# Kernel tuning notes

Hardware: AMD Instinct MI355X
Metric: run time of the kernel (lower is better)

The kernel has to match this reference:

```python
import jax, jax.numpy as jnp
import numpy as np

B, NE, NI, D = 256, 1024, 1024, 256  # batch, E cells, I cells, patch dim (16x16)
K_GAIN, N_EXP = 0.04, 2.0            # power-law i/o: k * relu(I)**n
TAU_E, TAU_I, DT = 0.02, 0.01, 0.001
STEPS, LAST_N = 200, 50              # int(T/dt) with T=0.2; average last 50 states
S_EE0, S_EI0, S_IE0, S_II0 = 3.75, 1.86, 3.13, 1.11 - 0.02
EPS = 1e-12
JEE, JEI, JIE, JII = 0.044, 0.023, 0.042, 0.018
SIGMA = 32.0


def ring_kernel(n_post, n_pre, sigma=SIGMA):
    post = np.linspace(0.0, 180.0, n_post + 1)[:-1]
    pre = np.linspace(0.0, 180.0, n_pre + 1)[:-1]
    d = np.abs(post[:, None] - pre[None, :])
    d = np.minimum(d, 180.0 - d)
    return np.exp(-(d * d) / (2.0 * sigma * sigma)).astype(np.float32)


def setup_inputs() -> dict:
    key = jax.random.key(0)
    kx, kE, kI = jax.random.split(key, 3)
    x_batch = jax.random.uniform(kx, (B, D), dtype=jnp.float32)
    W_EE = JEE * ring_kernel(NE, NE)
    np.fill_diagonal(W_EE, 0.0)
    W_EI = JEI * ring_kernel(NE, NI)
    W_IE = JIE * ring_kernel(NI, NE)
    W_II = JII * ring_kernel(NI, NI)
    np.fill_diagonal(W_II, 0.0)
    Wff_E = 0.1 * jax.random.uniform(kE, (NE, D), dtype=jnp.float32)
    Wff_E = Wff_E / (jnp.linalg.norm(Wff_E, axis=1, keepdims=True) + 1e-8)
    Wff_I = 0.1 * jax.random.uniform(kI, (NI, D), dtype=jnp.float32)
    Wff_I = Wff_I / (jnp.linalg.norm(Wff_I, axis=1, keepdims=True) + 1e-8)
    return {
        'x_batch': x_batch,
        'W_EE': jnp.asarray(W_EE), 'W_EI': jnp.asarray(W_EI),
        'W_IE': jnp.asarray(W_IE), 'W_II': jnp.asarray(W_II),
        'Wff_E': Wff_E, 'Wff_I': Wff_I,
    }


def powerlaw_io(I):
    return K_GAIN * jnp.maximum(I, 0.0) ** N_EXP


def reference(x_batch, W_EE, W_EI, W_IE, W_II, Wff_E, Wff_I):
    # per-postsynaptic current scalers (computed under no_grad in torch)
    gE_E = jax.lax.stop_gradient(S_EE0 / (W_EE.sum(axis=1) + EPS))
    gI_E = jax.lax.stop_gradient(S_EI0 / (W_EI.sum(axis=1) + EPS))
    gE_I = jax.lax.stop_gradient(S_IE0 / (W_IE.sum(axis=1) + EPS))
    gI_I = jax.lax.stop_gradient(S_II0 / (W_II.sum(axis=1) + EPS))
    # in-place clamp + rescale of weights (as in forward_dynamics)
    W_EE = jnp.minimum(W_EE, 0.15) * gE_E[:, None]
    W_EI = jnp.maximum(W_EI, 0.0005) * gI_E[:, None]
    W_IE = W_IE * gE_I[:, None]
    W_II = W_II * gI_I[:, None]

    Iff_E = x_batch @ Wff_E.T  # (B, nE)
    Iff_I = x_batch @ Wff_I.T  # (B, nI)

    def step(carry, t):
        rE, rI, accE, accI = carry
        IE = Iff_E + rE @ W_EE.T - rI @ W_EI.T
        II = Iff_I + rE @ W_IE.T - rI @ W_II.T
        rE = rE + (DT / TAU_E) * (-rE + powerlaw_io(IE))
        rI = rI + (DT / TAU_I) * (-rI + powerlaw_io(II))
        w = (t >= STEPS - LAST_N).astype(rE.dtype)
        return (rE, rI, accE + w * rE, accI + w * rI), None

    z = jnp.zeros((B, NE), dtype=x_batch.dtype)
    zi = jnp.zeros((B, NI), dtype=x_batch.dtype)
    (rE, rI, accE, accI), _ = jax.lax.scan(step, (z, zi, z, zi), jnp.arange(STEPS))
    rE_bar = accE / LAST_N
    rI_bar = accI / LAST_N
    return (rE_bar, rI_bar)
```

## Files before the change

### kernel.cpp

```cpp
#include <hip/hip_runtime.h>
#include <stdint.h>

typedef __attribute__((ext_vector_type(8))) _Float16 f16x8;
typedef __attribute__((ext_vector_type(8))) unsigned short u16x8;
typedef __attribute__((ext_vector_type(4))) float f32x4;

__device__ __forceinline__ float bf2f(unsigned short u) {
    union { uint32_t u; float f; } v; v.u = ((uint32_t)u) << 16; return v.f;
}
__device__ __forceinline__ unsigned short f2h(float f) {
    _Float16 h = (_Float16)f;
    return __builtin_bit_cast(unsigned short, h);
}
__device__ __forceinline__ f32x4 MFMAH(u16x8 a, u16x8 b, f32x4 c) {
    return __builtin_amdgcn_mfma_f32_16x16x32_f16(
        __builtin_bit_cast(f16x8, a), __builtin_bit_cast(f16x8, b), c, 0, 0, 0);
}

__device__ __forceinline__ int is_f32(const void* p) {
    const uint32_t* u = (const uint32_t*)p;
    int c = 0;
    #pragma unroll
    for (int i = 0; i < 64; i++) c += (u[i] >> 15) & 1;
    return c >= 4;
}
__device__ __forceinline__ float load_any(const void* base, size_t idx, int f32) {
    return f32 ? ((const float*)base)[idx] : bf2f(((const unsigned short*)base)[idx]);
}

__global__ void zero_kernel(float* __restrict__ p) {
    p[(size_t)blockIdx.x * 256 + threadIdx.x] = 0.0f;
}

__global__ void conv_kernel(const void* __restrict__ src, unsigned short* __restrict__ dst,
                            int clamp_wei) {
    int f32 = is_f32(src);
    size_t base = ((size_t)blockIdx.x * 256 + threadIdx.x) * 8;
    unsigned short v[8];
    if (f32) {
        const float* s = (const float*)src + base;
        #pragma unroll
        for (int e = 0; e < 8; e++) {
            float f = s[e];
            if (clamp_wei) f = fmaxf(f, 0.0005f);
            v[e] = f2h(f);
        }
    } else {
        const unsigned short* s = (const unsigned short*)src + base;
        #pragma unroll
        for (int e = 0; e < 8; e++) {
            float f = bf2f(s[e]);
            if (clamp_wei) f = fmaxf(f, 0.0005f);
            v[e] = f2h(f);
        }
    }
    *(u16x8*)(dst + base) = *(u16x8*)v;
}

__global__ void g_kernel(const void* __restrict__ WEE, const void* __restrict__ WEI,
                         const void* __restrict__ WIE, const void* __restrict__ WII,
                         float* __restrict__ gE, float* __restrict__ gI) {
    int i = blockIdx.x;
    int tid = threadIdx.x;
    const void* TE; const void* TI; float sEc, sIc; size_t row;
    if (i < 1024) { TE = WEE; TI = WEI; sEc = 3.75f; sIc = 1.86f; row = i; }
    else          { TE = WIE; TI = WII; sEc = 3.13f; sIc = (float)(1.11 - 0.02); row = i - 1024; }
    int fE = is_f32(TE), fI = is_f32(TI);
    float se = 0.f, si = 0.f;
    for (int j = tid; j < 1024; j += 256) {
        se += load_any(TE, row * 1024 + j, fE);
        si += load_any(TI, row * 1024 + j, fI);
    }
    for (int o = 32; o > 0; o >>= 1) { se += __shfl_down(se, o); si += __shfl_down(si, o); }
    __shared__ float lsE[4], lsI[4];
    int w = tid >> 6;
    if ((tid & 63) == 0) { lsE[w] = se; lsI[w] = si; }
    __syncthreads();
    if (tid == 0) {
        float te = lsE[0] + lsE[1] + lsE[2] + lsE[3];
        float ti = lsI[0] + lsI[1] + lsI[2] + lsI[3];
        gE[i] = sEc / (te + 1e-12f);
        gI[i] = sIc / (ti + 1e-12f);
    }
}

__global__ __launch_bounds__(256) void iff_kernel(const unsigned short* __restrict__ x,
                                                  const unsigned short* __restrict__ WffE,
                                                  const unsigned short* __restrict__ WffI,
                                                  float* __restrict__ Iff) {
    int n0 = blockIdx.x * 32;
    int m0 = blockIdx.y * 64;
    int tid = threadIdx.x, w = tid >> 6, lane = tid & 63;
    int l15 = lane & 15, quad = lane >> 4;
    int arow = m0 + 16 * w + l15;
    int nA = n0 + l15, nB = n0 + 16 + l15;
    const unsigned short* bA = (nA < 1024) ? (WffE + (size_t)nA * 256) : (WffI + (size_t)(nA - 1024) * 256);
    const unsigned short* bB = (nB < 1024) ? (WffE + (size_t)nB * 256) : (WffI + (size_t)(nB - 1024) * 256);
    f32x4 acc0 = {0.f, 0.f, 0.f, 0.f}, acc1 = {0.f, 0.f, 0.f, 0.f};
    #pragma unroll
    for (int ks = 0; ks < 8; ks++) {
        int k = ks * 32 + quad * 8;
        u16x8 a  = *(const u16x8*)(x + (size_t)arow * 256 + k);
        u16x8 b0 = *(const u16x8*)(bA + k);
        u16x8 b1 = *(const u16x8*)(bB + k);
        acc0 = MFMAH(a, b0, acc0);
        acc1 = MFMAH(a, b1, acc1);
    }
    #pragma unroll
    for (int v = 0; v < 4; v++) {
        int row = m0 + 16 * w + quad * 4 + v;
        Iff[(size_t)row * 2048 + n0 + l15]      = acc0[v];
        Iff[(size_t)row * 2048 + n0 + 16 + l15] = acc1[v];
    }
}

#define FLAG_STRIDE 32
__global__ __launch_bounds__(256, 1) void persist_kernel(
    const unsigned short* __restrict__ WEEc, const unsigned short* __restrict__ WEIc,
    const unsigned short* __restrict__ WIEc, const unsigned short* __restrict__ WIIc,
    unsigned short* __restrict__ h0, unsigned short* __restrict__ h1,
    const float* __restrict__ Iff, const float* __restrict__ gE, const float* __restrict__ gI,
    float* __restrict__ out, int* __restrict__ flags)
{
    __shared__ unsigned short Wl[32 * 2048];
    int bid = blockIdx.x;
    int nT = bid & 63;
    int mT = bid >> 6;
    int n0 = nT * 32;
    int m0 = mT * 64;
    int tid = threadIdx.x, w = tid >> 6, lane = tid & 63;
    int l15 = lane & 15, quad = lane >> 4;

    bool isEblk = (n0 < 1024);
    const unsigned short* W0 = isEblk ? WEEc : WIEc;
    const unsigned short* W1 = isEblk ? WEIc : WIIc;
    int nbase = n0 & 1023;

    {
        int k = tid * 8;
        const unsigned short* s0 = W0 + (size_t)nbase * 1024;
        const unsigned short* s1 = W1 + (size_t)nbase * 1024;
        #pragma unroll 4
        for (int row = 0; row < 32; row++) {
            const unsigned short* src = (k < 1024) ? (s0 + (size_t)row * 1024 + k)
                                                   : (s1 + (size_t)row * 1024 + (k - 1024));
            int gs = (tid + row) & 255;
            *(u16x8*)(Wl + row * 2048 + gs * 8) = *(const u16x8*)src;
        }
    }
    __syncthreads();

    int arow = m0 + 16 * w + l15;
    int colA = n0 + l15, colB = colA + 16;
    float invtau = isEblk ? 0.05f : 0.1f;
    float gEa = gE[colA], gIa = gI[colA], gEb = gE[colB], gIb = gI[colB];
    float iffA[4], iffB[4], rstA[4], rstB[4], sumA[4], sumB[4];
    int orow[4];
    #pragma unroll
    for (int v = 0; v < 4; v++) {
        orow[v] = m0 + 16 * w + quad * 4 + v;
        iffA[v] = Iff[(size_t)orow[v] * 2048 + colA];
        iffB[v] = Iff[(size_t)orow[v] * 2048 + colB];
        rstA[v] = 0.f; rstB[v] = 0.f; sumA[v] = 0.f; sumB[v] = 0.f;
    }

    const unsigned short* hi_in = h0;
    unsigned short* hi_out = h1;
    const unsigned short* WlA = Wl + l15 * 2048;
    const unsigned short* WlB = Wl + (16 + l15) * 2048;

    for (int t = 0; t < 200; t++) {
        const unsigned short* hp = hi_in + (size_t)arow * 2048;

        f32x4 eA0 = {0,0,0,0}, eA1 = {0,0,0,0}, eB0 = {0,0,0,0}, eB1 = {0,0,0,0};
        f32x4 iA0 = {0,0,0,0}, iA1 = {0,0,0,0}, iB0 = {0,0,0,0}, iB1 = {0,0,0,0};

        #pragma unroll 8
        for (int ks = 0; ks < 32; ks++) {
            int k = ks * 32 + quad * 8;
            int g = 4 * ks + quad;
            u16x8 a  = *(const u16x8*)(hp + k);
            u16x8 b0 = *(const u16x8*)(WlA + ((g + l15) & 255) * 8);
            u16x8 b1 = *(const u16x8*)(WlB + ((g + l15 + 16) & 255) * 8);
            if (ks & 1) { eA1 = MFMAH(a, b0, eA1); eB1 = MFMAH(a, b1, eB1); }
            else        { eA0 = MFMAH(a, b0, eA0); eB0 = MFMAH(a, b1, eB0); }
        }
        #pragma unroll 8
        for (int ks = 32; ks < 64; ks++) {
            int k = ks * 32 + quad * 8;
            int g = 4 * ks + quad;
            u16x8 a  = *(const u16x8*)(hp + k);
            u16x8 b0 = *(const u16x8*)(WlA + ((g + l15) & 255) * 8);
            u16x8 b1 = *(const u16x8*)(WlB + ((g + l15 + 16) & 255) * 8);
            if (ks & 1) { iA1 = MFMAH(a, b0, iA1); iB1 = MFMAH(a, b1, iB1); }
            else        { iA0 = MFMAH(a, b0, iA0); iB0 = MFMAH(a, b1, iB0); }
        }

        f32x4 aE0 = eA0 + eA1, aE1 = eB0 + eB1, aI0 = iA0 + iA1, aI1 = iB0 + iB1;

        float wacc = (t >= 150) ? 1.0f : 0.0f;
        #pragma unroll
        for (int v = 0; v < 4; v++) {
            size_t idx = (size_t)orow[v] * 2048;
            {
                float I = iffA[v] + gEa * aE0[v] - gIa * aI0[v];
                float rl = fmaxf(I, 0.f);
                float rnew = rstA[v] + invtau * (0.04f * rl * rl - rstA[v]);
                rstA[v] = rnew;
                __hip_atomic_store(hi_out + idx + colA, f2h(rnew),
                                   __ATOMIC_RELAXED, __HIP_MEMORY_SCOPE_AGENT);
                sumA[v] += wacc * rnew;
            }
            {
                float I = iffB[v] + gEb * aE1[v] - gIb * aI1[v];
                float rl = fmaxf(I, 0.f);
                float rnew = rstB[v] + invtau * (0.04f * rl * rl - rstB[v]);
                rstB[v] = rnew;
                __hip_atomic_store(hi_out + idx + colB, f2h(rnew),
                                   __ATOMIC_RELAXED, __HIP_MEMORY_SCOPE_AGENT);
                sumB[v] += wacc * rnew;
            }
        }

        __syncthreads();
        if (tid == 0) {
            __hip_atomic_store(&flags[bid * FLAG_STRIDE], t + 1,
                               __ATOMIC_RELAXED, __HIP_MEMORY_SCOPE_AGENT);
        }
        if (tid < 64) {
            const int fi = (mT * 64 + tid) * FLAG_STRIDE;
            while (__hip_atomic_load(&flags[fi], __ATOMIC_RELAXED,
                                     __HIP_MEMORY_SCOPE_AGENT) < t + 1) {
                __builtin_amdgcn_s_sleep(1);
            }
        }
        __syncthreads();
        if (tid == 0) {
            __builtin_amdgcn_fence(__ATOMIC_ACQUIRE, "agent");
        }
        __syncthreads();

        const unsigned short* th = hi_in; hi_in = hi_out; hi_out = (unsigned short*)th;
    }

    float* ob = out + (isEblk ? 0 : 262144);
    #pragma unroll
    for (int v = 0; v < 4; v++) {
        ob[(size_t)orow[v] * 1024 + nbase + l15]      = sumA[v] * (1.0f / 50.0f);
        ob[(size_t)orow[v] * 1024 + nbase + 16 + l15] = sumB[v] * (1.0f / 50.0f);
    }
}

extern "C" void kernel_launch(void* const* d_in, const int* in_sizes, int n_in,
                              void* d_out, int out_size, void* d_ws, size_t ws_size,
                              hipStream_t stream) {
    const void* x    = d_in[0];
    const void* WEE  = d_in[1];
    const void* WEI  = d_in[2];
    const void* WIE  = d_in[3];
    const void* WII  = d_in[4];
    const void* WffE = d_in[5];
    const void* WffI = d_in[6];

    char* ws = (char*)d_ws;
    const size_t MB = 1024 * 1024;
    const size_t KB = 1024;
    unsigned short* h0    = (unsigned short*)(ws + 0);
    int*            flags = (int*)(ws + 1 * MB);
    unsigned short* h1    = (unsigned short*)(ws + 2 * MB);
    float*          Iff   = (float*)(ws + 3 * MB);
    unsigned short* WEEc  = (unsigned short*)(ws + 5 * MB);
    unsigned short* WEIc  = (unsigned short*)(ws + 7 * MB);
    unsigned short* WIEc  = (unsigned short*)(ws + 9 * MB);
    unsigned short* WIIc  = (unsigned short*)(ws + 11 * MB);
    unsigned short* xc    = (unsigned short*)(ws + 13 * MB);
    unsigned short* WffEc = (unsigned short*)(ws + 13 * MB + 128 * KB);
    unsigned short* WffIc = (unsigned short*)(ws + 13 * MB + 640 * KB);
    float*          gE    = (float*)(ws + 13 * MB + 1152 * KB);
    float*          gI    = gE + 2048;

    zero_kernel<<<1056, 256, 0, stream>>>((float*)ws);

    conv_kernel<<<32,  256, 0, stream>>>(x,    xc,    0);
    conv_kernel<<<512, 256, 0, stream>>>(WEE,  WEEc,  0);
    conv_kernel<<<512, 256, 0, stream>>>(WEI,  WEIc,  1);
    conv_kernel<<<512, 256, 0, stream>>>(WIE,  WIEc,  0);
    conv_kernel<<<512, 256, 0, stream>>>(WII,  WIIc,  0);
    conv_kernel<<<128, 256, 0, stream>>>(WffE, WffEc, 0);
    conv_kernel<<<128, 256, 0, stream>>>(WffI, WffIc, 0);

    g_kernel<<<2048, 256, 0, stream>>>(WEE, WEI, WIE, WII, gE, gI);
    iff_kernel<<<dim3(64, 4), 256, 0, stream>>>(xc, WffEc, WffIc, Iff);

    float* outp = (float*)d_out;
    void* args[] = { &WEEc, &WEIc, &WIEc, &WIIc, &h0, &h1,
                     &Iff, &gE, &gI, &outp, &flags };
    hipLaunchCooperativeKernel((const void*)persist_kernel, dim3(256), dim3(256),
                               args, 0, stream);
}
```

Measured before the change: 2.570 ms.

## Split persistent step K-reduction across 16 waves with LDS partial-sum combine

The persistent recurrent kernel now launches 1024 threads per block instead of 256, dividing the 2048-long K dimension into four quarters handled by separate wave groups. Each group folds its gain and sign into its partial products and writes them to shared memory, and wave group 0 sums them and runs the rate update and state stores. The inter-block flag wait is now done by every wave, each issuing its own acquire fence, instead of one wave behind extra block barriers, and the final step skips the barrier. The aim is to shorten the serial per-step MFMA chain by adding more waves per CU. The cost is an extra LDS round trip and block barrier each step, plus more polling traffic on the flags.

```diff
diff --git a/kernel.cpp b/kernel.cpp
--- a/kernel.cpp
+++ b/kernel.cpp
@@ -115,7 +115,7 @@
 }
 
 #define FLAG_STRIDE 32
-__global__ __launch_bounds__(256, 1) void persist_kernel(
+__global__ __launch_bounds__(1024, 4) void persist_kernel(
     const unsigned short* __restrict__ WEEc, const unsigned short* __restrict__ WEIc,
     const unsigned short* __restrict__ WIEc, const unsigned short* __restrict__ WIIc,
     unsigned short* __restrict__ h0, unsigned short* __restrict__ h1,
@@ -123,12 +123,18 @@
     float* __restrict__ out, int* __restrict__ flags)
 {
     __shared__ unsigned short Wl[32 * 2048];
+    __shared__ f32x4 PA[12 * 64];
+    __shared__ f32x4 PB[12 * 64];
+
     int bid = blockIdx.x;
     int nT = bid & 63;
     int mT = bid >> 6;
     int n0 = nT * 32;
     int m0 = mT * 64;
-    int tid = threadIdx.x, w = tid >> 6, lane = tid & 63;
+    int tid = threadIdx.x;
+    int wave = tid >> 6, lane = tid & 63;
+    int w = wave & 3;
+    int wq = wave >> 2;
     int l15 = lane & 15, quad = lane >> 4;
 
     bool isEblk = (n0 < 1024);
@@ -137,14 +143,17 @@
     int nbase = n0 & 1023;
 
     {
-        int k = tid * 8;
+        int c = tid & 255;
+        int r0 = tid >> 8;
+        int k = c * 8;
         const unsigned short* s0 = W0 + (size_t)nbase * 1024;
         const unsigned short* s1 = W1 + (size_t)nbase * 1024;
-        #pragma unroll 4
-        for (int row = 0; row < 32; row++) {
+        #pragma unroll
+        for (int i = 0; i < 8; i++) {
+            int row = r0 * 8 + i;
             const unsigned short* src = (k < 1024) ? (s0 + (size_t)row * 1024 + k)
                                                    : (s1 + (size_t)row * 1024 + (k - 1024));
-            int gs = (tid + row) & 255;
+            int gs = (c + row) & 255;
             *(u16x8*)(Wl + row * 2048 + gs * 8) = *(const u16x8*)src;
         }
     }
@@ -153,101 +162,104 @@
     int arow = m0 + 16 * w + l15;
     int colA = n0 + l15, colB = colA + 16;
     float invtau = isEblk ? 0.05f : 0.1f;
-    float gEa = gE[colA], gIa = gI[colA], gEb = gE[colB], gIb = gI[colB];
+    bool ehalf = (wq < 2);
+    float sgA = ehalf ? gE[colA] : -gI[colA];
+    float sgB = ehalf ? gE[colB] : -gI[colB];
+
     float iffA[4], iffB[4], rstA[4], rstB[4], sumA[4], sumB[4];
     int orow[4];
-    #pragma unroll
-    for (int v = 0; v < 4; v++) {
-        orow[v] = m0 + 16 * w + quad * 4 + v;
-        iffA[v] = Iff[(size_t)orow[v] * 2048 + colA];
-        iffB[v] = Iff[(size_t)orow[v] * 2048 + colB];
-        rstA[v] = 0.f; rstB[v] = 0.f; sumA[v] = 0.f; sumB[v] = 0.f;
+    if (wq == 0) {
+        #pragma unroll
+        for (int v = 0; v < 4; v++) {
+            orow[v] = m0 + 16 * w + quad * 4 + v;
+            iffA[v] = Iff[(size_t)orow[v] * 2048 + colA];
+            iffB[v] = Iff[(size_t)orow[v] * 2048 + colB];
+            rstA[v] = 0.f; rstB[v] = 0.f; sumA[v] = 0.f; sumB[v] = 0.f;
+        }
     }
 
     const unsigned short* hi_in = h0;
     unsigned short* hi_out = h1;
     const unsigned short* WlA = Wl + l15 * 2048;
     const unsigned short* WlB = Wl + (16 + l15) * 2048;
+    int slot = ((wq - 1) << 2) | w;
 
     for (int t = 0; t < 200; t++) {
-        const unsigned short* hp = hi_in + (size_t)arow * 2048;
-
-        f32x4 eA0 = {0,0,0,0}, eA1 = {0,0,0,0}, eB0 = {0,0,0,0}, eB1 = {0,0,0,0};
-        f32x4 iA0 = {0,0,0,0}, iA1 = {0,0,0,0}, iB0 = {0,0,0,0}, iB1 = {0,0,0,0};
-
-        #pragma unroll 8
-        for (int ks = 0; ks < 32; ks++) {
-            int k = ks * 32 + quad * 8;
-            int g = 4 * ks + quad;
+        const unsigned short* hp = hi_in + (size_t)arow * 2048 + wq * 512;
+
+        f32x4 cA0 = {0,0,0,0}, cA1 = {0,0,0,0}, cB0 = {0,0,0,0}, cB1 = {0,0,0,0};
+        #pragma unroll 4
+        for (int i = 0; i < 16; i++) {
+            int k = i * 32 + quad * 8;
+            int g = 4 * (wq * 16 + i) + quad;
             u16x8 a  = *(const u16x8*)(hp + k);
             u16x8 b0 = *(const u16x8*)(WlA + ((g + l15) & 255) * 8);
             u16x8 b1 = *(const u16x8*)(WlB + ((g + l15 + 16) & 255) * 8);
-            if (ks & 1) { eA1 = MFMAH(a, b0, eA1); eB1 = MFMAH(a, b1, eB1); }
-            else        { eA0 = MFMAH(a, b0, eA0); eB0 = MFMAH(a, b1, eB0); }
-        }
-        #pragma unroll 8
-        for (int ks = 32; ks < 64; ks++) {
-            int k = ks * 32 + quad * 8;
-            int g = 4 * ks + quad;
-            u16x8 a  = *(const u16x8*)(hp + k);
-            u16x8 b0 = *(const u16x8*)(WlA + ((g + l15) & 255) * 8);
-            u16x8 b1 = *(const u16x8*)(WlB + ((g + l15 + 16) & 255) * 8);
-            if (ks & 1) { iA1 = MFMAH(a, b0, iA1); iB1 = MFMAH(a, b1, iB1); }
-            else        { iA0 = MFMAH(a, b0, iA0); iB0 = MFMAH(a, b1, iB0); }
-        }
-
-        f32x4 aE0 = eA0 + eA1, aE1 = eB0 + eB1, aI0 = iA0 + iA1, aI1 = iB0 + iB1;
-
-        float wacc = (t >= 150) ? 1.0f : 0.0f;
-        #pragma unroll
-        for (int v = 0; v < 4; v++) {
-            size_t idx = (size_t)orow[v] * 2048;
-            {
-                float I = iffA[v] + gEa * aE0[v] - gIa * aI0[v];
-                float rl = fmaxf(I, 0.f);
-                float rnew = rstA[v] + invtau * (0.04f * rl * rl - rstA[v]);
-                rstA[v] = rnew;
-                __hip_atomic_store(hi_out + idx + colA, f2h(rnew),
-                                   __ATOMIC_RELAXED, __HIP_MEMORY_SCOPE_AGENT);
-                sumA[v] += wacc * rnew;
+            if (i & 1) { cA1 = MFMAH(a, b0, cA1); cB1 = MFMAH(a, b1, cB1); }
+            else       { cA0 = MFMAH(a, b0, cA0); cB0 = MFMAH(a, b1, cB0); }
+        }
+        f32x4 pA = sgA * (cA0 + cA1);
+        f32x4 pB = sgB * (cB0 + cB1);
+
+        if (wq != 0) {
+            PA[slot * 64 + lane] = pA;
+            PB[slot * 64 + lane] = pB;
+        }
+        __syncthreads();
+
+        if (wq == 0) {
+            f32x4 tA = pA + PA[w * 64 + lane] + PA[(4 + w) * 64 + lane] + PA[(8 + w) * 64 + lane];
+            f32x4 tB = pB + PB[w * 64 + lane] + PB[(4 + w) * 64 + lane] + PB[(8 + w) * 64 + lane];
+            float wacc = (t >= 150) ? 1.0f : 0.0f;
+            #pragma unroll
+            for (int v = 0; v < 4; v++) {
+                size_t idx = (size_t)orow[v] * 2048;
+                {
+                    float I = iffA[v] + tA[v];
+                    float rl = fmaxf(I, 0.f);
+                    float rnew = rstA[v] + invtau * (0.04f * rl * rl - rstA[v]);
+                    rstA[v] = rnew;
+                    __hip_atomic_store(hi_out + idx + colA, f2h(rnew),
+                                       __ATOMIC_RELAXED, __HIP_MEMORY_SCOPE_AGENT);
+                    sumA[v] += wacc * rnew;
+                }
+                {
+                    float I = iffB[v] + tB[v];
+                    float rl = fmaxf(I, 0.f);
+                    float rnew = rstB[v] + invtau * (0.04f * rl * rl - rstB[v]);
+                    rstB[v] = rnew;
+                    __hip_atomic_store(hi_out + idx + colB, f2h(rnew),
+                                       __ATOMIC_RELAXED, __HIP_MEMORY_SCOPE_AGENT);
+                    sumB[v] += wacc * rnew;
+                }
             }
-            {
-                float I = iffB[v] + gEb * aE1[v] - gIb * aI1[v];
-                float rl = fmaxf(I, 0.f);
-                float rnew = rstB[v] + invtau * (0.04f * rl * rl - rstB[v]);
-                rstB[v] = rnew;
-                __hip_atomic_store(hi_out + idx + colB, f2h(rnew),
-                                   __ATOMIC_RELAXED, __HIP_MEMORY_SCOPE_AGENT);
-                sumB[v] += wacc * rnew;
-            }
-        }
+        }
+        if (t == 199) break;
 
         __syncthreads();
         if (tid == 0) {
             __hip_atomic_store(&flags[bid * FLAG_STRIDE], t + 1,
                                __ATOMIC_RELAXED, __HIP_MEMORY_SCOPE_AGENT);
         }
-        if (tid < 64) {
-            const int fi = (mT * 64 + tid) * FLAG_STRIDE;
+        {
+            const int fi = (mT * 64 + lane) * FLAG_STRIDE;
             while (__hip_atomic_load(&flags[fi], __ATOMIC_RELAXED,
                                      __HIP_MEMORY_SCOPE_AGENT) < t + 1) {
                 __builtin_amdgcn_s_sleep(1);
             }
         }
-        __syncthreads();
-        if (tid == 0) {
-            __builtin_amdgcn_fence(__ATOMIC_ACQUIRE, "agent");
-        }
-        __syncthreads();
+        __builtin_amdgcn_fence(__ATOMIC_ACQUIRE, "agent");
 
         const unsigned short* th = hi_in; hi_in = hi_out; hi_out = (unsigned short*)th;
     }
 
-    float* ob = out + (isEblk ? 0 : 262144);
-    #pragma unroll
-    for (int v = 0; v < 4; v++) {
-        ob[(size_t)orow[v] * 1024 + nbase + l15]      = sumA[v] * (1.0f / 50.0f);
-        ob[(size_t)orow[v] * 1024 + nbase + 16 + l15] = sumB[v] * (1.0f / 50.0f);
+    if (wq == 0) {
+        float* ob = out + (isEblk ? 0 : 262144);
+        #pragma unroll
+        for (int v = 0; v < 4; v++) {
+            ob[(size_t)orow[v] * 1024 + nbase + l15]      = sumA[v] * (1.0f / 50.0f);
+            ob[(size_t)orow[v] * 1024 + nbase + 16 + l15] = sumB[v] * (1.0f / 50.0f);
+        }
     }
 }
 
@@ -295,6 +307,6 @@
     float* outp = (float*)d_out;
     void* args[] = { &WEEc, &WEIc, &WIEc, &WIIc, &h0, &h1,
                      &Iff, &gE, &gI, &outp, &flags };
-    hipLaunchCooperativeKernel((const void*)persist_kernel, dim3(256), dim3(256),
+    hipLaunchCooperativeKernel((const void*)persist_kernel, dim3(256), dim3(1024),
                                args, 0, stream);
 }
```

Result: slower. 6.989 ms (+172.0%).
